# Optimization experiments

Measured on AMD Instinct MI355X. Metric: run time of the kernel, lower is better.

## Reference

```python
import jax, jax.numpy as jnp
import numpy as np

H = 64
N_NODES = 12000
N_EDGES = 50000


def setup_inputs() -> dict:
    key = jax.random.key(0)
    ks = jax.random.split(key, 16)
    s = 1.0 / np.sqrt(H)
    inp = {
        "node": jax.random.normal(ks[0], (N_NODES, H), jnp.float32),
        "edge": jax.random.normal(ks[1], (N_EDGES, H), jnp.float32),
        "hidden_feats": jax.random.normal(ks[2], (N_NODES, H), jnp.float32),
        "src": jax.random.randint(ks[3], (N_EDGES,), 0, N_NODES, jnp.int32),
        "dst": jax.random.randint(ks[4], (N_EDGES,), 0, N_NODES, jnp.int32),
        # edge_network: Linear(H, 2H) -> ReLU -> Linear(2H, H*H)
        "W1": jax.random.uniform(ks[5], (2 * H, H), jnp.float32, -s, s),
        "b1": jax.random.uniform(ks[6], (2 * H,), jnp.float32, -s, s),
        "W2": jax.random.uniform(ks[7], (H * H, 2 * H), jnp.float32, -1 / np.sqrt(2 * H), 1 / np.sqrt(2 * H)),
        "b2": jax.random.uniform(ks[8], (H * H,), jnp.float32, -1 / np.sqrt(2 * H), 1 / np.sqrt(2 * H)),
        # GRUCell params (torch layout: [3H, H], gate order r,z,n)
        "W_ih": jax.random.uniform(ks[9], (3 * H, H), jnp.float32, -s, s),
        "W_hh": jax.random.uniform(ks[10], (3 * H, H), jnp.float32, -s, s),
        "b_ih": jax.random.uniform(ks[11], (3 * H,), jnp.float32, -s, s),
        "b_hh": jax.random.uniform(ks[12], (3 * H,), jnp.float32, -s, s),
        # LayerNorm params
        "gamma": jnp.ones((H,), jnp.float32),
        "beta": jnp.zeros((H,), jnp.float32),
    }
    return inp


def _gru_cell(x, h, W_ih, W_hh, b_ih, b_hh):
    gi = x @ W_ih.T + b_ih  # [N, 3H]
    gh = h @ W_hh.T + b_hh  # [N, 3H]
    r = jax.nn.sigmoid(gi[:, :H] + gh[:, :H])
    z = jax.nn.sigmoid(gi[:, H:2 * H] + gh[:, H:2 * H])
    n = jnp.tanh(gi[:, 2 * H:] + r * gh[:, 2 * H:])
    return (1.0 - z) * n + z * h


def reference(node, edge, hidden_feats, src, dst, W1, b1, W2, b2,
              W_ih, W_hh, b_ih, b_hh, gamma, beta):
    n_nodes = node.shape[0]
    # edge network -> per-edge [H,H] weight matrices
    eh = jax.nn.relu(edge @ W1.T + b1)                      # [E, 2H]
    Wedge = (eh @ W2.T + b2).reshape(-1, H, H)              # [E, H, H]
    # gather src feats, per-edge matmul (row-vector @ matrix), scatter-sum to dst
    msg = jnp.einsum('eh,ehk->ek', node[src], Wedge)        # [E, H]
    agg = jax.ops.segment_sum(msg, dst, num_segments=n_nodes)  # [N, H]
    new_node_feats = jax.nn.relu(agg)
    out = _gru_cell(new_node_feats, hidden_feats, W_ih, W_hh, b_ih, b_hh)
    # LayerNorm (eps=1e-5)
    mu = jnp.mean(out, axis=-1, keepdims=True)
    var = jnp.var(out, axis=-1, keepdims=True)
    out = (out - mu) * jax.lax.rsqrt(var + 1e-5) * gamma + beta
    return out
```

## Files before the change

### kernel.cpp

```cpp
#include <hip/hip_runtime.h>

#define H 64
#define NEDGE 50000
#define NNODE 12000
#define EPAD 50176

typedef _Float16 f16;
typedef _Float16 h8 __attribute__((ext_vector_type(8)));
typedef float f4 __attribute__((ext_vector_type(4)));

#define O_EDGEH 0ull
#define O_W2G   6422528ull
#define O_W1G   7471104ull
#define O_NB    7487488ull
#define O_AGG   10559488ull
#define O_WTIH  13631488ull
#define O_WTHH  13680640ull

__device__ __forceinline__ void async16(const void* g, void* l) {
  __builtin_amdgcn_global_load_lds((const __attribute__((address_space(1))) void*)g,
                                   (__attribute__((address_space(3))) void*)l, 16, 0, 0);
}

__global__ __launch_bounds__(256) void k_prep(const float* __restrict__ edge, const float* __restrict__ W1,
                                              const float* __restrict__ W2, const float* __restrict__ b2,
                                              const float* __restrict__ node,
                                              const float* __restrict__ Wih, const float* __restrict__ Whh,
                                              f16* __restrict__ edgeh, f16* __restrict__ w1g, f16* __restrict__ w2g,
                                              float* __restrict__ nb, float* __restrict__ wtih, float* __restrict__ wthh) {
  __shared__ float bs[64][65];
  __shared__ float xs[64][65];
  int bid = blockIdx.x;
  if (bid < 14720) {
    int id = bid * 256 + threadIdx.x;
    if (id < 3211264) {
      edgeh[id] = (id < NEDGE * 64) ? (f16)edge[id] : (f16)0.f;
      return;
    }
    id -= 3211264;
    if (id < 524288) {
      int ii = id & 7, l = (id >> 3) & 63, t4 = (id >> 9) & 3, s = (id >> 11) & 3, h = id >> 13;
      int n = t4 * 16 + (l & 15), j = s * 32 + ((l >> 4) << 3) + ii;
      w2g[id] = (f16)W2[(h * 64 + n) * 128 + j];
      return;
    }
    id -= 524288;
    if (id < 8192) {
      int ii = id & 7, l = (id >> 3) & 63, tt = (id >> 9) & 7, s = id >> 12;
      int n = tt * 16 + (l & 15), k = s * 32 + ((l >> 4) << 3) + ii;
      w1g[id] = (f16)W1[n * 64 + k];
      return;
    }
    id -= 8192;
    if (id < 12288) {
      int k = id / 192, g = id % 192;
      wtih[id] = Wih[g * 64 + k];
      return;
    }
    id -= 12288;
    if (id < 12288) {
      int k = id / 192, g = id % 192;
      wthh[id] = Whh[g * 64 + k];
    }
    return;
  }
  int t = threadIdx.x;
  int n0 = (bid - 14720) * 64;
#pragma unroll
  for (int it = 0; it < 16; ++it) {
    int idx = t + it * 256;
    int rr = idx >> 6, cc = idx & 63;
    bs[rr][cc] = b2[idx];
    int nn = n0 + rr;
    xs[rr][cc] = (nn < NNODE) ? node[(long)nn * 64 + cc] : 0.f;
  }
  __syncthreads();
  int f0 = (t & 15) * 4, e0 = (t >> 4) * 4;
  float acc[4][4] = {};
#pragma unroll 4
  for (int k = 0; k < 64; ++k) {
    f4 w = *(const f4*)&bs[k][f0];
#pragma unroll
    for (int i = 0; i < 4; ++i) {
      float x = xs[e0 + i][k];
      acc[i][0] = fmaf(x, w[0], acc[i][0]); acc[i][1] = fmaf(x, w[1], acc[i][1]);
      acc[i][2] = fmaf(x, w[2], acc[i][2]); acc[i][3] = fmaf(x, w[3], acc[i][3]);
    }
  }
#pragma unroll
  for (int i = 0; i < 4; ++i) {
    int nn = n0 + e0 + i;
    if (nn < NNODE)
#pragma unroll
      for (int j = 0; j < 4; ++j) nb[(long)nn * 64 + f0 + j] = acc[i][j];
  }
}

__global__ __launch_bounds__(256, 2) void k_msg(const float* __restrict__ node,
                                                const int* __restrict__ src, const int* __restrict__ dst,
                                                const f16* __restrict__ edgeh, const f16* __restrict__ w1g,
                                                const f16* __restrict__ w2g, const float* __restrict__ b1,
                                                const float* __restrict__ nb, float* __restrict__ agg) {
  __shared__ __align__(16) char lds[67072];
  f16* est = (f16*)lds;
  f16* eh_s = (f16*)(lds + 16384);
  f16* bbuf = (f16*)lds;
  f16* vT = (f16*)(lds + 49152);
  int* ssrc = (int*)(lds + 65536);
  int* sdst = (int*)(lds + 66048);
  float* b1s = (float*)(lds + 66560);

  int t = threadIdx.x;
  int e_base = blockIdx.x * 128;

  if (t < 128) {
    int eg = e_base + t;
    bool valid = eg < NEDGE;
    ssrc[t] = valid ? src[eg] : 0;
    sdst[t] = valid ? dst[eg] : 0;
  } else {
    b1s[t - 128] = b1[t - 128];
  }
  {
    const char* ehb = (const char*)edgeh;
#pragma unroll
    for (int r = 0; r < 4; ++r) {
      int idx = r * 256 + t;
      int e = idx >> 3, c1 = idx & 7;
      int c = c1 ^ (e & 7);
      async16(ehb + ((long)(e_base + e) * 8 + c) * 16, (char*)est + idx * 16);
    }
  }
  {
    int e = t >> 1, half = t & 1;
    int eg = e_base + e;
    int si = (eg < NEDGE) ? src[eg] : 0;
    const f4* nr = (const f4*)(node + (long)si * 64 + half * 32);
#pragma unroll
    for (int b = 0; b < 8; ++b) {
      f4 vv = nr[b];
#pragma unroll
      for (int m = 0; m < 4; ++m) vT[(half * 32 + b * 4 + m) * 128 + e] = (f16)vv[m];
    }
  }
  __syncthreads();

  int wave = t >> 6, lane = t & 63;
  int mh = wave & 1, nh = wave >> 1;
  int l15 = lane & 15, lq = lane >> 4;

  h8 afr[4][2];
#pragma unroll
  for (int g = 0; g < 4; ++g) {
    int eg = mh * 64 + g * 16 + l15;
#pragma unroll
    for (int s = 0; s < 2; ++s) {
      int c = (s * 4 + lq) ^ (eg & 7);
      afr[g][s] = *(const h8*)(est + (eg * 8 + c) * 8);
    }
  }
  h8 bfr[2][4];
#pragma unroll
  for (int s = 0; s < 2; ++s)
#pragma unroll
    for (int tt = 0; tt < 4; ++tt)
      bfr[s][tt] = *(const h8*)(w1g + ((s * 8 + nh * 4 + tt) * 64 + lane) * 8);
  f4 acc_eh[4][4];
#pragma unroll
  for (int g = 0; g < 4; ++g)
#pragma unroll
    for (int tt = 0; tt < 4; ++tt) acc_eh[g][tt] = (f4){0.f, 0.f, 0.f, 0.f};
#pragma unroll
  for (int s = 0; s < 2; ++s)
#pragma unroll
    for (int g = 0; g < 4; ++g)
#pragma unroll
      for (int tt = 0; tt < 4; ++tt)
        acc_eh[g][tt] = __builtin_amdgcn_mfma_f32_16x16x32_f16(afr[g][s], bfr[s][tt], acc_eh[g][tt], 0, 0, 0);
  __syncthreads();

  const char* w2b = (const char*)w2g;
#pragma unroll
  for (int r = 0; r < 4; ++r) async16(w2b + r * 4096 + t * 16, (char*)bbuf + r * 4096 + t * 16);

#pragma unroll
  for (int g = 0; g < 4; ++g)
#pragma unroll
    for (int tt = 0; tt < 4; ++tt) {
      int n = nh * 64 + tt * 16 + l15;
      int jg = n >> 3;
#pragma unroll
      for (int r = 0; r < 4; ++r) {
        int e = mh * 64 + g * 16 + lq * 4 + r;
        float val = fmaxf(acc_eh[g][tt][r] + b1s[n], 0.f);
        eh_s[(e * 16 + (jg ^ (e & 15))) * 8 + (n & 7)] = (f16)val;
      }
    }
  __syncthreads();

  h8 ehreg[4][4];
#pragma unroll
  for (int g = 0; g < 4; ++g) {
    int eg = mh * 64 + g * 16 + l15;
#pragma unroll
    for (int s = 0; s < 4; ++s) {
      int jg = (s * 4 + lq) ^ (eg & 15);
      ehreg[g][s] = *(const h8*)(eh_s + (eg * 16 + jg) * 8);
    }
  }
  __syncthreads();

  f4 acc[4][2];
#pragma unroll
  for (int g = 0; g < 4; ++g) {
    acc[g][0] = (f4){0.f, 0.f, 0.f, 0.f};
    acc[g][1] = (f4){0.f, 0.f, 0.f, 0.f};
  }
  for (int h = 0; h < 64; ++h) {
    __syncthreads();
    {
      const char* gsrc = w2b + (h + 1) * 16384;
      char* ldst = (char*)bbuf + ((h + 1) & 1) * 16384;
#pragma unroll
      for (int r = 0; r < 4; ++r) async16(gsrc + r * 4096 + t * 16, ldst + r * 4096 + t * 16);
    }
    const f16* bb = bbuf + (h & 1) * 8192;
    f16 vh[4];
#pragma unroll
    for (int g = 0; g < 4; ++g) vh[g] = vT[h * 128 + mh * 64 + g * 16 + l15];
#pragma unroll
    for (int s = 0; s < 4; ++s) {
      h8 bf0 = *(const h8*)(bb + ((s * 4 + nh * 2) * 64 + lane) * 8);
      h8 bf1 = *(const h8*)(bb + ((s * 4 + nh * 2 + 1) * 64 + lane) * 8);
#pragma unroll
      for (int g = 0; g < 4; ++g) {
        h8 a = ehreg[g][s] * vh[g];
        acc[g][0] = __builtin_amdgcn_mfma_f32_16x16x32_f16(a, bf0, acc[g][0], 0, 0, 0);
        acc[g][1] = __builtin_amdgcn_mfma_f32_16x16x32_f16(a, bf1, acc[g][1], 0, 0, 0);
      }
    }
  }

#pragma unroll
  for (int g = 0; g < 4; ++g)
#pragma unroll
    for (int t2 = 0; t2 < 2; ++t2)
#pragma unroll
      for (int r = 0; r < 4; ++r) {
        int el = mh * 64 + g * 16 + lq * 4 + r;
        if (e_base + el < NEDGE) {
          int n = nh * 32 + t2 * 16 + l15;
          float v = acc[g][t2][r] + nb[(long)ssrc[el] * 64 + n];
          atomicAdd(&agg[(long)sdst[el] * 64 + n], v);
        }
      }
}

__global__ __launch_bounds__(256) void k_node(const float* __restrict__ agg, const float* __restrict__ hid,
                                              const float* __restrict__ wtih, const float* __restrict__ wthh,
                                              const float* __restrict__ bih, const float* __restrict__ bhh,
                                              const float* __restrict__ gamma, const float* __restrict__ beta,
                                              float* __restrict__ out) {
  int t = threadIdx.x;
  int wave = t >> 6, lane = t & 63;
  int n0 = blockIdx.x * 32 + wave * 8;
  float x[8], hv[8];
#pragma unroll
  for (int i = 0; i < 8; ++i) {
    x[i] = fmaxf(agg[(long)(n0 + i) * 64 + lane], 0.f);
    hv[i] = hid[(long)(n0 + i) * 64 + lane];
  }
  float gir[8] = {0}, giz[8] = {0}, gin[8] = {0}, ghr[8] = {0}, ghz[8] = {0}, ghn[8] = {0};
  for (int k = 0; k < 64; ++k) {
    float wi0 = wtih[k * 192 + lane], wi1 = wtih[k * 192 + 64 + lane], wi2 = wtih[k * 192 + 128 + lane];
    float wh0 = wthh[k * 192 + lane], wh1 = wthh[k * 192 + 64 + lane], wh2 = wthh[k * 192 + 128 + lane];
#pragma unroll
    for (int i = 0; i < 8; ++i) {
      float xk = __shfl(x[i], k);
      float hk = __shfl(hv[i], k);
      gir[i] = fmaf(wi0, xk, gir[i]); giz[i] = fmaf(wi1, xk, giz[i]); gin[i] = fmaf(wi2, xk, gin[i]);
      ghr[i] = fmaf(wh0, hk, ghr[i]); ghz[i] = fmaf(wh1, hk, ghz[i]); ghn[i] = fmaf(wh2, hk, ghn[i]);
    }
  }
  float bir = bih[lane], biz = bih[64 + lane], bin = bih[128 + lane];
  float bhr = bhh[lane], bhz = bhh[64 + lane], bhn = bhh[128 + lane];
  float gam = gamma[lane], bet = beta[lane];
#pragma unroll
  for (int i = 0; i < 8; ++i) {
    float r = 1.f / (1.f + __expf(-(gir[i] + bir + ghr[i] + bhr)));
    float z = 1.f / (1.f + __expf(-(giz[i] + biz + ghz[i] + bhz)));
    float nn = tanhf(gin[i] + bin + r * (ghn[i] + bhn));
    float o = (1.f - z) * nn + z * hv[i];
    float s = o, s2 = o * o;
#pragma unroll
    for (int d = 1; d < 64; d <<= 1) {
      s += __shfl_xor(s, d);
      s2 += __shfl_xor(s2, d);
    }
    float mu = s * (1.f / 64.f);
    float var = s2 * (1.f / 64.f) - mu * mu;
    out[(long)(n0 + i) * 64 + lane] = (o - mu) * rsqrtf(var + 1e-5f) * gam + bet;
  }
}

extern "C" void kernel_launch(void* const* d_in, const int* in_sizes, int n_in,
                              void* d_out, int out_size, void* d_ws, size_t ws_size,
                              hipStream_t stream) {
  const float* node = (const float*)d_in[0];
  const float* edge = (const float*)d_in[1];
  const float* hid = (const float*)d_in[2];
  const int* src = (const int*)d_in[3];
  const int* dst = (const int*)d_in[4];
  const float* W1 = (const float*)d_in[5];
  const float* b1 = (const float*)d_in[6];
  const float* W2 = (const float*)d_in[7];
  const float* b2 = (const float*)d_in[8];
  const float* Wih = (const float*)d_in[9];
  const float* Whh = (const float*)d_in[10];
  const float* bih = (const float*)d_in[11];
  const float* bhh = (const float*)d_in[12];
  const float* gamma = (const float*)d_in[13];
  const float* beta = (const float*)d_in[14];

  char* ws = (char*)d_ws;
  f16* edgeh = (f16*)(ws + O_EDGEH);
  f16* w2g = (f16*)(ws + O_W2G);
  f16* w1g = (f16*)(ws + O_W1G);
  float* nb = (float*)(ws + O_NB);
  float* agg = (float*)(ws + O_AGG);
  float* wtih = (float*)(ws + O_WTIH);
  float* wthh = (float*)(ws + O_WTHH);

  hipMemsetAsync(agg, 0, (size_t)NNODE * 64 * sizeof(float), stream);
  k_prep<<<14908, 256, 0, stream>>>(edge, W1, W2, b2, node, Wih, Whh, edgeh, w1g, w2g, nb, wtih, wthh);
  k_msg<<<391, 256, 0, stream>>>(node, src, dst, edgeh, w1g, w2g, b1, nb, agg);
  k_node<<<375, 256, 0, stream>>>(agg, hid, wtih, wthh, bih, bhh, gamma, beta, (float*)d_out);
}
```

Measured before the change: 213.9 us.

## Rework message kernel tiling, vectorize prep, and move GRU matmuls to MFMA

The edge-conversion prep now converts eight floats per thread with vector loads instead of one element per thread. The message kernel switches to 64-edge blocks where each wave owns 16 output columns. It streams W2 fragments straight from global memory into registers with a one-step register prefetch, replacing the LDS double buffer, its per-step barriers and the old vT layout. The GRU+LayerNorm kernel now uses fp16 MFMA on a fused [x|h] x [Wih;Whh] weight packed in prep, replacing scalar FMA loops with shuffles. The GRU inputs and weights are rounded to fp16, which adds precision risk, and W2 fragments are re-read from global memory by every block.

```diff
diff --git a/kernel.cpp b/kernel.cpp
--- a/kernel.cpp
+++ b/kernel.cpp
@@ -12,10 +12,9 @@
 #define O_EDGEH 0ull
 #define O_W2G   6422528ull
 #define O_W1G   7471104ull
-#define O_NB    7487488ull
-#define O_AGG   10559488ull
-#define O_WTIH  13631488ull
-#define O_WTHH  13680640ull
+#define O_WG    7487488ull
+#define O_NB    7553024ull
+#define O_AGG   10625024ull
 
 __device__ __forceinline__ void async16(const void* g, void* l) {
   __builtin_amdgcn_global_load_lds((const __attribute__((address_space(1))) void*)g,
@@ -27,45 +26,51 @@
                                               const float* __restrict__ node,
                                               const float* __restrict__ Wih, const float* __restrict__ Whh,
                                               f16* __restrict__ edgeh, f16* __restrict__ w1g, f16* __restrict__ w2g,
-                                              float* __restrict__ nb, float* __restrict__ wtih, float* __restrict__ wthh) {
+                                              f16* __restrict__ wg, float* __restrict__ nb) {
+  int bid = blockIdx.x;
+  int t = threadIdx.x;
+  if (bid < 1568) {
+    long id8 = (long)bid * 256 + t;
+    long e = id8 >> 3;
+    int c = (int)(id8 & 7) * 8;
+    h8 o = {};
+    if (e < NEDGE) {
+      const float* p = edge + e * 64 + c;
+      f4 v0 = *(const f4*)p, v1 = *(const f4*)(p + 4);
+#pragma unroll
+      for (int j = 0; j < 4; ++j) { o[j] = (f16)v0[j]; o[4 + j] = (f16)v1[j]; }
+    }
+    *(h8*)(edgeh + e * 64 + c) = o;
+    return;
+  }
+  if (bid < 3616) {
+    int id = (bid - 1568) * 256 + t;
+    int ii = id & 7, l = (id >> 3) & 63, t4 = (id >> 9) & 3, s = (id >> 11) & 3, h = id >> 13;
+    int n = t4 * 16 + (l & 15), j = s * 32 + ((l >> 4) << 3) + ii;
+    w2g[id] = (f16)W2[(h * 64 + n) * 128 + j];
+    return;
+  }
+  if (bid < 3648) {
+    int id = (bid - 3616) * 256 + t;
+    int ii = id & 7, l = (id >> 3) & 63, tt = (id >> 9) & 7, s = id >> 12;
+    int n = tt * 16 + (l & 15), k = s * 32 + ((l >> 4) << 3) + ii;
+    w1g[id] = (f16)W1[n * 64 + k];
+    return;
+  }
+  if (bid < 3776) {
+    int id = (bid - 3648) * 256 + t;
+    int ii = id & 7, l = (id >> 3) & 63, tt = (id >> 9) & 15, s = id >> 13;
+    int k = s * 32 + ((l >> 4) << 3) + ii, n = tt * 16 + (l & 15);
+    float v;
+    if (n < 128) v = (k < 64) ? Wih[n * 64 + k] : Whh[n * 64 + (k - 64)];
+    else if (n < 192) v = (k < 64) ? Wih[n * 64 + k] : 0.f;
+    else v = (k < 64) ? 0.f : Whh[(n - 64) * 64 + (k - 64)];
+    wg[id] = (f16)v;
+    return;
+  }
   __shared__ float bs[64][65];
   __shared__ float xs[64][65];
-  int bid = blockIdx.x;
-  if (bid < 14720) {
-    int id = bid * 256 + threadIdx.x;
-    if (id < 3211264) {
-      edgeh[id] = (id < NEDGE * 64) ? (f16)edge[id] : (f16)0.f;
-      return;
-    }
-    id -= 3211264;
-    if (id < 524288) {
-      int ii = id & 7, l = (id >> 3) & 63, t4 = (id >> 9) & 3, s = (id >> 11) & 3, h = id >> 13;
-      int n = t4 * 16 + (l & 15), j = s * 32 + ((l >> 4) << 3) + ii;
-      w2g[id] = (f16)W2[(h * 64 + n) * 128 + j];
-      return;
-    }
-    id -= 524288;
-    if (id < 8192) {
-      int ii = id & 7, l = (id >> 3) & 63, tt = (id >> 9) & 7, s = id >> 12;
-      int n = tt * 16 + (l & 15), k = s * 32 + ((l >> 4) << 3) + ii;
-      w1g[id] = (f16)W1[n * 64 + k];
-      return;
-    }
-    id -= 8192;
-    if (id < 12288) {
-      int k = id / 192, g = id % 192;
-      wtih[id] = Wih[g * 64 + k];
-      return;
-    }
-    id -= 12288;
-    if (id < 12288) {
-      int k = id / 192, g = id % 192;
-      wthh[id] = Whh[g * 64 + k];
-    }
-    return;
-  }
-  int t = threadIdx.x;
-  int n0 = (bid - 14720) * 64;
+  int n0 = (bid - 3776) * 64;
 #pragma unroll
   for (int it = 0; it < 16; ++it) {
     int idx = t + it * 256;
@@ -96,35 +101,32 @@
   }
 }
 
-__global__ __launch_bounds__(256, 2) void k_msg(const float* __restrict__ node,
+__global__ __launch_bounds__(256, 3) void k_msg(const float* __restrict__ node,
                                                 const int* __restrict__ src, const int* __restrict__ dst,
                                                 const f16* __restrict__ edgeh, const f16* __restrict__ w1g,
                                                 const f16* __restrict__ w2g, const float* __restrict__ b1,
-                                                const float* __restrict__ nb, float* __restrict__ agg) {
-  __shared__ __align__(16) char lds[67072];
-  f16* est = (f16*)lds;
-  f16* eh_s = (f16*)(lds + 16384);
-  f16* bbuf = (f16*)lds;
-  f16* vT = (f16*)(lds + 49152);
-  int* ssrc = (int*)(lds + 65536);
-  int* sdst = (int*)(lds + 66048);
-  float* b1s = (float*)(lds + 66560);
+                                                const float* __restrict__ nbt, float* __restrict__ agg) {
+  __shared__ __align__(16) f16 est[64 * 8 * 8];
+  __shared__ __align__(16) f16 eh_s[64 * 16 * 8];
+  __shared__ __align__(16) f16 vT2[64 * 8 * 8];
+  __shared__ int ssrc[64];
+  __shared__ int sdst[64];
+  __shared__ float b1s[128];
 
   int t = threadIdx.x;
-  int e_base = blockIdx.x * 128;
-
-  if (t < 128) {
+  int e_base = blockIdx.x * 64;
+
+  if (t < 64) {
     int eg = e_base + t;
     bool valid = eg < NEDGE;
     ssrc[t] = valid ? src[eg] : 0;
     sdst[t] = valid ? dst[eg] : 0;
-  } else {
-    b1s[t - 128] = b1[t - 128];
-  }
+  }
+  if (t >= 128) b1s[t - 128] = b1[t - 128];
   {
     const char* ehb = (const char*)edgeh;
 #pragma unroll
-    for (int r = 0; r < 4; ++r) {
+    for (int r = 0; r < 2; ++r) {
       int idx = r * 256 + t;
       int e = idx >> 3, c1 = idx & 7;
       int c = c1 ^ (e & 7);
@@ -132,175 +134,229 @@
     }
   }
   {
-    int e = t >> 1, half = t & 1;
+    int e = t >> 2, q = t & 3;
     int eg = e_base + e;
     int si = (eg < NEDGE) ? src[eg] : 0;
-    const f4* nr = (const f4*)(node + (long)si * 64 + half * 32);
-#pragma unroll
-    for (int b = 0; b < 8; ++b) {
-      f4 vv = nr[b];
-#pragma unroll
-      for (int m = 0; m < 4; ++m) vT[(half * 32 + b * 4 + m) * 128 + e] = (f16)vv[m];
-    }
+    const f4* nr = (const f4*)(node + (long)si * 64 + q * 16);
+    f4 a0 = nr[0], a1 = nr[1], a2 = nr[2], a3 = nr[3];
+    h8 p0, p1;
+#pragma unroll
+    for (int m = 0; m < 4; ++m) {
+      p0[m] = (f16)a0[m]; p0[4 + m] = (f16)a1[m];
+      p1[m] = (f16)a2[m]; p1[4 + m] = (f16)a3[m];
+    }
+    int g0 = (q * 2) ^ (e & 7), g1 = (q * 2 + 1) ^ (e & 7);
+    *(h8*)(vT2 + (e * 8 + g0) * 8) = p0;
+    *(h8*)(vT2 + (e * 8 + g1) * 8) = p1;
   }
   __syncthreads();
 
   int wave = t >> 6, lane = t & 63;
-  int mh = wave & 1, nh = wave >> 1;
   int l15 = lane & 15, lq = lane >> 4;
 
-  h8 afr[4][2];
+  {
+    h8 afr[4][2];
+#pragma unroll
+    for (int g = 0; g < 4; ++g) {
+      int e = g * 16 + l15;
+#pragma unroll
+      for (int s = 0; s < 2; ++s) {
+        int c = (s * 4 + lq) ^ (e & 7);
+        afr[g][s] = *(const h8*)(est + (e * 8 + c) * 8);
+      }
+    }
+    h8 bfr[2][2];
+#pragma unroll
+    for (int s = 0; s < 2; ++s)
+#pragma unroll
+      for (int j = 0; j < 2; ++j)
+        bfr[s][j] = *(const h8*)(w1g + ((s * 8 + wave * 2 + j) * 64 + lane) * 8);
+    f4 acc_eh[4][2];
+#pragma unroll
+    for (int g = 0; g < 4; ++g) { acc_eh[g][0] = (f4){0,0,0,0}; acc_eh[g][1] = (f4){0,0,0,0}; }
+#pragma unroll
+    for (int s = 0; s < 2; ++s)
+#pragma unroll
+      for (int g = 0; g < 4; ++g)
+#pragma unroll
+        for (int j = 0; j < 2; ++j)
+          acc_eh[g][j] = __builtin_amdgcn_mfma_f32_16x16x32_f16(afr[g][s], bfr[s][j], acc_eh[g][j], 0, 0, 0);
+#pragma unroll
+    for (int g = 0; g < 4; ++g)
+#pragma unroll
+      for (int j = 0; j < 2; ++j) {
+        int n = wave * 32 + j * 16 + l15;
+        int jg = n >> 3;
+#pragma unroll
+        for (int r = 0; r < 4; ++r) {
+          int e = g * 16 + lq * 4 + r;
+          float val = fmaxf(acc_eh[g][j][r] + b1s[n], 0.f);
+          eh_s[(e * 16 + (jg ^ (e & 15))) * 8 + (n & 7)] = (f16)val;
+        }
+      }
+  }
+  __syncthreads();
+
+  h8 ehreg[4][4];
 #pragma unroll
   for (int g = 0; g < 4; ++g) {
-    int eg = mh * 64 + g * 16 + l15;
-#pragma unroll
-    for (int s = 0; s < 2; ++s) {
-      int c = (s * 4 + lq) ^ (eg & 7);
-      afr[g][s] = *(const h8*)(est + (eg * 8 + c) * 8);
-    }
-  }
-  h8 bfr[2][4];
-#pragma unroll
-  for (int s = 0; s < 2; ++s)
-#pragma unroll
-    for (int tt = 0; tt < 4; ++tt)
-      bfr[s][tt] = *(const h8*)(w1g + ((s * 8 + nh * 4 + tt) * 64 + lane) * 8);
-  f4 acc_eh[4][4];
+    int e = g * 16 + l15;
+#pragma unroll
+    for (int s = 0; s < 4; ++s) {
+      int jg = (s * 4 + lq) ^ (e & 15);
+      ehreg[g][s] = *(const h8*)(eh_s + (e * 16 + jg) * 8);
+    }
+  }
+
+  f4 acc[4];
+#pragma unroll
+  for (int g = 0; g < 4; ++g) acc[g] = (f4){0.f, 0.f, 0.f, 0.f};
+
+  const char* w2b = (const char*)w2g + wave * 1024 + lane * 16;
+  h8 cur0 = *(const h8*)(w2b);
+  h8 cur1 = *(const h8*)(w2b + 4096);
+  h8 cur2 = *(const h8*)(w2b + 8192);
+  h8 cur3 = *(const h8*)(w2b + 12288);
+
+#pragma unroll 1
+  for (int hb = 0; hb < 8; ++hb) {
+    h8 vh8[4];
+#pragma unroll
+    for (int g = 0; g < 4; ++g) {
+      int e = g * 16 + l15;
+      vh8[g] = *(const h8*)(vT2 + (e * 8 + (hb ^ (e & 7))) * 8);
+    }
+#pragma unroll
+    for (int hh = 0; hh < 8; ++hh) {
+      int h = hb * 8 + hh;
+      const char* gp = w2b + (long)(h + 1) * 16384;
+      h8 pf0 = *(const h8*)(gp);
+      h8 pf1 = *(const h8*)(gp + 4096);
+      h8 pf2 = *(const h8*)(gp + 8192);
+      h8 pf3 = *(const h8*)(gp + 12288);
+      f16 vs;
+#pragma unroll
+      for (int g = 0; g < 4; ++g) {
+        vs = vh8[g][hh];
+        h8 a = ehreg[g][0] * vs;
+        acc[g] = __builtin_amdgcn_mfma_f32_16x16x32_f16(a, cur0, acc[g], 0, 0, 0);
+        a = ehreg[g][1] * vs;
+        acc[g] = __builtin_amdgcn_mfma_f32_16x16x32_f16(a, cur1, acc[g], 0, 0, 0);
+        a = ehreg[g][2] * vs;
+        acc[g] = __builtin_amdgcn_mfma_f32_16x16x32_f16(a, cur2, acc[g], 0, 0, 0);
+        a = ehreg[g][3] * vs;
+        acc[g] = __builtin_amdgcn_mfma_f32_16x16x32_f16(a, cur3, acc[g], 0, 0, 0);
+      }
+      cur0 = pf0; cur1 = pf1; cur2 = pf2; cur3 = pf3;
+    }
+  }
+
+  int n = wave * 16 + l15;
 #pragma unroll
   for (int g = 0; g < 4; ++g)
 #pragma unroll
-    for (int tt = 0; tt < 4; ++tt) acc_eh[g][tt] = (f4){0.f, 0.f, 0.f, 0.f};
-#pragma unroll
-  for (int s = 0; s < 2; ++s)
-#pragma unroll
-    for (int g = 0; g < 4; ++g)
-#pragma unroll
-      for (int tt = 0; tt < 4; ++tt)
-        acc_eh[g][tt] = __builtin_amdgcn_mfma_f32_16x16x32_f16(afr[g][s], bfr[s][tt], acc_eh[g][tt], 0, 0, 0);
-  __syncthreads();
-
-  const char* w2b = (const char*)w2g;
-#pragma unroll
-  for (int r = 0; r < 4; ++r) async16(w2b + r * 4096 + t * 16, (char*)bbuf + r * 4096 + t * 16);
-
-#pragma unroll
-  for (int g = 0; g < 4; ++g)
-#pragma unroll
-    for (int tt = 0; tt < 4; ++tt) {
-      int n = nh * 64 + tt * 16 + l15;
-      int jg = n >> 3;
-#pragma unroll
-      for (int r = 0; r < 4; ++r) {
-        int e = mh * 64 + g * 16 + lq * 4 + r;
-        float val = fmaxf(acc_eh[g][tt][r] + b1s[n], 0.f);
-        eh_s[(e * 16 + (jg ^ (e & 15))) * 8 + (n & 7)] = (f16)val;
-      }
-    }
-  __syncthreads();
-
-  h8 ehreg[4][4];
-#pragma unroll
-  for (int g = 0; g < 4; ++g) {
-    int eg = mh * 64 + g * 16 + l15;
-#pragma unroll
-    for (int s = 0; s < 4; ++s) {
-      int jg = (s * 4 + lq) ^ (eg & 15);
-      ehreg[g][s] = *(const h8*)(eh_s + (eg * 16 + jg) * 8);
-    }
-  }
-  __syncthreads();
-
-  f4 acc[4][2];
-#pragma unroll
-  for (int g = 0; g < 4; ++g) {
-    acc[g][0] = (f4){0.f, 0.f, 0.f, 0.f};
-    acc[g][1] = (f4){0.f, 0.f, 0.f, 0.f};
-  }
-  for (int h = 0; h < 64; ++h) {
-    __syncthreads();
-    {
-      const char* gsrc = w2b + (h + 1) * 16384;
-      char* ldst = (char*)bbuf + ((h + 1) & 1) * 16384;
-#pragma unroll
-      for (int r = 0; r < 4; ++r) async16(gsrc + r * 4096 + t * 16, ldst + r * 4096 + t * 16);
-    }
-    const f16* bb = bbuf + (h & 1) * 8192;
-    f16 vh[4];
-#pragma unroll
-    for (int g = 0; g < 4; ++g) vh[g] = vT[h * 128 + mh * 64 + g * 16 + l15];
-#pragma unroll
-    for (int s = 0; s < 4; ++s) {
-      h8 bf0 = *(const h8*)(bb + ((s * 4 + nh * 2) * 64 + lane) * 8);
-      h8 bf1 = *(const h8*)(bb + ((s * 4 + nh * 2 + 1) * 64 + lane) * 8);
-#pragma unroll
-      for (int g = 0; g < 4; ++g) {
-        h8 a = ehreg[g][s] * vh[g];
-        acc[g][0] = __builtin_amdgcn_mfma_f32_16x16x32_f16(a, bf0, acc[g][0], 0, 0, 0);
-        acc[g][1] = __builtin_amdgcn_mfma_f32_16x16x32_f16(a, bf1, acc[g][1], 0, 0, 0);
-      }
-    }
-  }
-
-#pragma unroll
-  for (int g = 0; g < 4; ++g)
-#pragma unroll
-    for (int t2 = 0; t2 < 2; ++t2)
-#pragma unroll
-      for (int r = 0; r < 4; ++r) {
-        int el = mh * 64 + g * 16 + lq * 4 + r;
-        if (e_base + el < NEDGE) {
-          int n = nh * 32 + t2 * 16 + l15;
-          float v = acc[g][t2][r] + nb[(long)ssrc[el] * 64 + n];
-          atomicAdd(&agg[(long)sdst[el] * 64 + n], v);
-        }
-      }
+    for (int r = 0; r < 4; ++r) {
+      int el = g * 16 + lq * 4 + r;
+      if (e_base + el < NEDGE) {
+        float v = acc[g][r] + nbt[(long)ssrc[el] * 64 + n];
+        atomicAdd(&agg[(long)sdst[el] * 64 + n], v);
+      }
+    }
 }
 
 __global__ __launch_bounds__(256) void k_node(const float* __restrict__ agg, const float* __restrict__ hid,
-                                              const float* __restrict__ wtih, const float* __restrict__ wthh,
+                                              const f16* __restrict__ wg,
                                               const float* __restrict__ bih, const float* __restrict__ bhh,
                                               const float* __restrict__ gamma, const float* __restrict__ beta,
                                               float* __restrict__ out) {
+  __shared__ __align__(16) f16 xh_s[128 * 136];
+  __shared__ float bsum[128], bin_s[64], bhn_s[64], gam_s[64], bet_s[64];
   int t = threadIdx.x;
+  int n0 = blockIdx.x * 128;
+
+  if (t < 128) bsum[t] = bih[t] + bhh[t];
+  else if (t < 192) bin_s[t - 128] = bih[t];
+  else bhn_s[t - 192] = bhh[t - 64];
+  if (t < 64) gam_s[t] = gamma[t];
+  else if (t < 128) bet_s[t - 64] = beta[t - 64];
+
+  {
+    int m = t >> 1, half = t & 1;
+    int mg = n0 + m;
+    bool vld = mg < NNODE;
+    const float* sp = half ? (hid + (long)mg * 64) : (agg + (long)mg * 64);
+#pragma unroll
+    for (int jj = 0; jj < 8; ++jj) {
+      f4 v0 = {0,0,0,0}, v1 = {0,0,0,0};
+      if (vld) { v0 = *(const f4*)(sp + jj * 8); v1 = *(const f4*)(sp + jj * 8 + 4); }
+      h8 pk;
+#pragma unroll
+      for (int m2 = 0; m2 < 4; ++m2) {
+        pk[m2] = (f16)(half ? v0[m2] : fmaxf(v0[m2], 0.f));
+        pk[4 + m2] = (f16)(half ? v1[m2] : fmaxf(v1[m2], 0.f));
+      }
+      *(h8*)(xh_s + m * 136 + half * 64 + jj * 8) = pk;
+    }
+  }
+  __syncthreads();
+
   int wave = t >> 6, lane = t & 63;
-  int n0 = blockIdx.x * 32 + wave * 8;
-  float x[8], hv[8];
-#pragma unroll
-  for (int i = 0; i < 8; ++i) {
-    x[i] = fmaxf(agg[(long)(n0 + i) * 64 + lane], 0.f);
-    hv[i] = hid[(long)(n0 + i) * 64 + lane];
-  }
-  float gir[8] = {0}, giz[8] = {0}, gin[8] = {0}, ghr[8] = {0}, ghz[8] = {0}, ghn[8] = {0};
-  for (int k = 0; k < 64; ++k) {
-    float wi0 = wtih[k * 192 + lane], wi1 = wtih[k * 192 + 64 + lane], wi2 = wtih[k * 192 + 128 + lane];
-    float wh0 = wthh[k * 192 + lane], wh1 = wthh[k * 192 + 64 + lane], wh2 = wthh[k * 192 + 128 + lane];
-#pragma unroll
-    for (int i = 0; i < 8; ++i) {
-      float xk = __shfl(x[i], k);
-      float hk = __shfl(hv[i], k);
-      gir[i] = fmaf(wi0, xk, gir[i]); giz[i] = fmaf(wi1, xk, giz[i]); gin[i] = fmaf(wi2, xk, gin[i]);
-      ghr[i] = fmaf(wh0, hk, ghr[i]); ghz[i] = fmaf(wh1, hk, ghz[i]); ghn[i] = fmaf(wh2, hk, ghn[i]);
-    }
-  }
-  float bir = bih[lane], biz = bih[64 + lane], bin = bih[128 + lane];
-  float bhr = bhh[lane], bhz = bhh[64 + lane], bhn = bhh[128 + lane];
-  float gam = gamma[lane], bet = beta[lane];
-#pragma unroll
-  for (int i = 0; i < 8; ++i) {
-    float r = 1.f / (1.f + __expf(-(gir[i] + bir + ghr[i] + bhr)));
-    float z = 1.f / (1.f + __expf(-(giz[i] + biz + ghz[i] + bhz)));
-    float nn = tanhf(gin[i] + bin + r * (ghn[i] + bhn));
-    float o = (1.f - z) * nn + z * hv[i];
-    float s = o, s2 = o * o;
-#pragma unroll
-    for (int d = 1; d < 64; d <<= 1) {
-      s += __shfl_xor(s, d);
-      s2 += __shfl_xor(s2, d);
-    }
-    float mu = s * (1.f / 64.f);
-    float var = s2 * (1.f / 64.f) - mu * mu;
-    out[(long)(n0 + i) * 64 + lane] = (o - mu) * rsqrtf(var + 1e-5f) * gam + bet;
-  }
+  int l15 = lane & 15, lq = lane >> 4;
+
+  f4 acc[2][16];
+#pragma unroll
+  for (int g = 0; g < 2; ++g)
+#pragma unroll
+    for (int tt = 0; tt < 16; ++tt) acc[g][tt] = (f4){0.f, 0.f, 0.f, 0.f};
+
+#pragma unroll
+  for (int s = 0; s < 4; ++s) {
+    h8 a0 = *(const h8*)(xh_s + (wave * 32 + l15) * 136 + s * 32 + lq * 8);
+    h8 a1 = *(const h8*)(xh_s + (wave * 32 + 16 + l15) * 136 + s * 32 + lq * 8);
+#pragma unroll
+    for (int tt = 0; tt < 16; ++tt) {
+      h8 b = *(const h8*)(wg + ((s * 16 + tt) * 64 + lane) * 8);
+      acc[0][tt] = __builtin_amdgcn_mfma_f32_16x16x32_f16(a0, b, acc[0][tt], 0, 0, 0);
+      acc[1][tt] = __builtin_amdgcn_mfma_f32_16x16x32_f16(a1, b, acc[1][tt], 0, 0, 0);
+    }
+  }
+
+#pragma unroll
+  for (int g = 0; g < 2; ++g)
+#pragma unroll
+    for (int r = 0; r < 4; ++r) {
+      int mg = n0 + wave * 32 + g * 16 + lq * 4 + r;
+      bool vld = mg < NNODE;
+      float o[4], ssum = 0.f, s2 = 0.f;
+#pragma unroll
+      for (int t0 = 0; t0 < 4; ++t0) {
+        int f = t0 * 16 + l15;
+        float rpre = acc[g][t0][r] + bsum[f];
+        float zpre = acc[g][4 + t0][r] + bsum[64 + f];
+        float ginv = acc[g][8 + t0][r] + bin_s[f];
+        float ghnv = acc[g][12 + t0][r] + bhn_s[f];
+        float rr = 1.f / (1.f + __expf(-rpre));
+        float zz = 1.f / (1.f + __expf(-zpre));
+        float hv = vld ? hid[(long)mg * 64 + f] : 0.f;
+        float nn = tanhf(ginv + rr * ghnv);
+        float oo = (1.f - zz) * nn + zz * hv;
+        o[t0] = oo; ssum += oo; s2 += oo * oo;
+      }
+#pragma unroll
+      for (int d = 1; d < 16; d <<= 1) {
+        ssum += __shfl_xor(ssum, d);
+        s2 += __shfl_xor(s2, d);
+      }
+      float mu = ssum * (1.f / 64.f);
+      float var = s2 * (1.f / 64.f) - mu * mu;
+      float rstd = rsqrtf(var + 1e-5f);
+      if (vld)
+#pragma unroll
+        for (int t0 = 0; t0 < 4; ++t0) {
+          int f = t0 * 16 + l15;
+          out[(long)mg * 64 + f] = (o[t0] - mu) * rstd * gam_s[f] + bet_s[f];
+        }
+    }
 }
 
 extern "C" void kernel_launch(void* const* d_in, const int* in_sizes, int n_in,
@@ -326,13 +382,12 @@
   f16* edgeh = (f16*)(ws + O_EDGEH);
   f16* w2g = (f16*)(ws + O_W2G);
   f16* w1g = (f16*)(ws + O_W1G);
+  f16* wg = (f16*)(ws + O_WG);
   float* nb = (float*)(ws + O_NB);
   float* agg = (float*)(ws + O_AGG);
-  float* wtih = (float*)(ws + O_WTIH);
-  float* wthh = (float*)(ws + O_WTHH);
 
   hipMemsetAsync(agg, 0, (size_t)NNODE * 64 * sizeof(float), stream);
-  k_prep<<<14908, 256, 0, stream>>>(edge, W1, W2, b2, node, Wih, Whh, edgeh, w1g, w2g, nb, wtih, wthh);
-  k_msg<<<391, 256, 0, stream>>>(node, src, dst, edgeh, w1g, w2g, b1, nb, agg);
-  k_node<<<375, 256, 0, stream>>>(agg, hid, wtih, wthh, bih, bhh, gamma, beta, (float*)d_out);
-}
+  k_prep<<<3964, 256, 0, stream>>>(edge, W1, W2, b2, node, Wih, Whh, edgeh, w1g, w2g, wg, nb);
+  k_msg<<<784, 256, 0, stream>>>(node, src, dst, edgeh, w1g, w2g, b1, nb, agg);
+  k_node<<<94, 256, 0, stream>>>(agg, hid, wg, bih, bhh, gamma, beta, (float*)d_out);
+}
```

Result: slower. 219.5 us (+2.6%).
